# Kernel optimization log

Measured on AMD Instinct MI355X. Metric: run time of the kernel, lower is better.

The kernel has to match this reference:

```python
import jax, jax.numpy as jnp
import numpy as np

B, L, D, H = 4, 2048, 1024, 16
HD = D // H
SCALE = 1.0 / (D / H) ** 0.5


def setup_inputs() -> dict:
    key = jax.random.key(0)
    ks = jax.random.split(key, 11)
    s = 1.0 / np.sqrt(D)
    return {
        "q": jax.random.normal(ks[0], (B, L, D), jnp.float32),
        "k": jax.random.normal(ks[1], (B, L, D), jnp.float32),
        "v": jax.random.normal(ks[2], (B, L, D), jnp.float32),
        "Wq": jax.random.normal(ks[3], (D, D), jnp.float32) * s,
        "bq": jnp.zeros((D,), jnp.float32),
        "Wk": jax.random.normal(ks[4], (D, D), jnp.float32) * s,
        "bk": jnp.zeros((D,), jnp.float32),
        "Wv": jax.random.normal(ks[5], (D, D), jnp.float32) * s,
        "bv": jnp.zeros((D,), jnp.float32),
        "Wo": jax.random.normal(ks[6], (D, D), jnp.float32) * s,
        "bo": jnp.zeros((D,), jnp.float32),
    }


def _split_heads(x):
    # [b, l, h*d] -> [b, h, l, d]
    b, l, _ = x.shape
    return x.reshape(b, l, H, HD).transpose(0, 2, 1, 3)


def reference(q, k, v, Wq, bq, Wk, bk, Wv, bv, Wo, bo):
    # Linear projections (torch Linear: x @ W.T + b)
    qh = _split_heads(q @ Wq.T + bq)            # [b, h, l, d]
    kh = _split_heads(k @ Wk.T + bk)            # [b, h, l, d]
    vh = _split_heads(v @ Wv.T + bv)            # [b, h, l, d]
    scores = jnp.einsum('bhqd,bhkd->bhqk', qh, kh) * SCALE
    attn = jax.nn.softmax(scores, axis=-1)       # dropout p=0 -> identity
    out = jnp.einsum('bhqk,bhkd->bhqd', attn, vh)
    out = out.transpose(0, 2, 1, 3).reshape(q.shape[0], q.shape[1], D)
    return out @ Wo.T + bo
```

## Files before the change

### kernel.cpp

```cpp
#include <hip/hip_runtime.h>


#define Bsz 4
#define Lq 2048
#define Dm 1024
#define NH 16
#define HD 64
#define QSCALE 0.18033688011112042f

typedef unsigned short u16;
typedef __attribute__((ext_vector_type(4))) short bf16x4;
typedef __attribute__((ext_vector_type(8))) short short8;
typedef __attribute__((ext_vector_type(4))) float f32x4;

#define MFMA32(a, b, c) __builtin_amdgcn_mfma_f32_16x16x32_bf16(a, b, c, 0, 0, 0)

typedef __attribute__((address_space(3))) unsigned su32;
typedef __attribute__((address_space(1))) unsigned gu32;
__device__ __forceinline__ void gl_lds16(const u16* g, u16* l) {
  __builtin_amdgcn_global_load_lds((gu32*)(g), (su32*)(l), 16, 0, 0);
}

__device__ __forceinline__ u16 f2b(float x) {
  unsigned u = __builtin_bit_cast(unsigned, x);
  return (u16)((u + 0x7fffu + ((u >> 16) & 1u)) >> 16);
}
__device__ __forceinline__ unsigned pk2(float a, float b) {
  return (unsigned)f2b(a) | ((unsigned)f2b(b) << 16);
}
__device__ __forceinline__ unsigned pk2p(float a, float b) {
  return __builtin_amdgcn_perm(__builtin_bit_cast(unsigned, b) + 0x8000u,
                               __builtin_bit_cast(unsigned, a) + 0x8000u, 0x07060302u);
}
__device__ __forceinline__ float fexp2(float x) {
#if __has_builtin(__builtin_amdgcn_exp2f)
  return __builtin_amdgcn_exp2f(x);
#else
  return exp2f(x);
#endif
}

__global__ void castk3(const float* __restrict__ q, const float* __restrict__ k,
                       const float* __restrict__ v, u16* __restrict__ dst) {
  const float* s = blockIdx.y == 0 ? q : (blockIdx.y == 1 ? k : v);
  u16* d = dst + (size_t)blockIdx.y * (Bsz * Lq * Dm);
  int i = (blockIdx.x * 256 + threadIdx.x) * 8;
  float4 a = *(const float4*)(s + i);
  float4 b = *(const float4*)(s + i + 4);
  short8 o;
  o[0] = (short)f2b(a.x); o[1] = (short)f2b(a.y);
  o[2] = (short)f2b(a.z); o[3] = (short)f2b(a.w);
  o[4] = (short)f2b(b.x); o[5] = (short)f2b(b.y);
  o[6] = (short)f2b(b.z); o[7] = (short)f2b(b.w);
  *(short8*)(d + i) = o;
}

__global__ void castw(const float* __restrict__ s0, const float* __restrict__ s1,
                      const float* __restrict__ s2, const float* __restrict__ s3,
                      u16* __restrict__ d0, u16* __restrict__ d1,
                      u16* __restrict__ d2, u16* __restrict__ d3) {
  const float* s; u16* d; float sc = 1.0f;
  switch (blockIdx.y) {
    case 0: s = s0; d = d0; sc = QSCALE; break;
    case 1: s = s1; d = d1; break;
    case 2: s = s2; d = d2; break;
    default: s = s3; d = d3; break;
  }
  int i = (blockIdx.x * 256 + threadIdx.x) * 8;
  float4 a = *(const float4*)(s + i);
  float4 b = *(const float4*)(s + i + 4);
  short8 o;
  o[0] = (short)f2b(a.x * sc); o[1] = (short)f2b(a.y * sc);
  o[2] = (short)f2b(a.z * sc); o[3] = (short)f2b(a.w * sc);
  o[4] = (short)f2b(b.x * sc); o[5] = (short)f2b(b.y * sc);
  o[6] = (short)f2b(b.z * sc); o[7] = (short)f2b(b.w * sc);
  *(short8*)(d + i) = o;
}

__global__ __launch_bounds__(256) void qkv_gemm(
    const u16* __restrict__ Ab,
    const u16* __restrict__ Wqb, const u16* __restrict__ Wkb, const u16* __restrict__ Wvb,
    const float* __restrict__ bq, const float* __restrict__ bk, const float* __restrict__ bv,
    u16* __restrict__ Qh, u16* __restrict__ Kh, u16* __restrict__ Vtg)
{
  __shared__ __align__(16) u16 As[128 * 32];
  __shared__ __align__(16) u16 Bs[128 * 32];
  const int z = blockIdx.z;
  const u16* A  = Ab + (size_t)z * (Bsz * Lq * Dm);
  const u16* Bt = z == 0 ? Wqb : (z == 1 ? Wkb : Wvb);
  const float* bias = z == 0 ? bq : (z == 1 ? bk : bv);
  const float bscale = z == 0 ? QSCALE : 1.0f;

  const int tid  = threadIdx.x;
  const int lane = tid & 63;
  const int wave = tid >> 6;
  const int quad = lane >> 4;
  const int r16  = lane & 15;
  const int wm   = (wave >> 1) * 64;
  const int wn   = (wave & 1) * 64;
  const int m0   = blockIdx.y * 128;
  const int n0   = blockIdx.x * 128;

  const u16* ga = A  + (size_t)(m0 + wave * 32 + (lane >> 2)) * Dm + (lane & 3) * 8;
  const u16* gb = Bt + (size_t)(n0 + wave * 32 + (lane >> 2)) * Dm + (lane & 3) * 8;
  u16* la = As + wave * 1024;
  u16* lb = Bs + wave * 1024;

  f32x4 acc[4][4] = {};

  for (int k0 = 0; k0 < Dm; k0 += 32) {
    gl_lds16(ga + k0, la);
    gl_lds16(ga + k0 + 16 * Dm, la + 512);
    gl_lds16(gb + k0, lb);
    gl_lds16(gb + k0 + 16 * Dm, lb + 512);
    __syncthreads();

    short8 af[4], bfr[4];
#pragma unroll
    for (int mt = 0; mt < 4; ++mt) af[mt]  = *(const short8*)&As[(wm + mt * 16 + r16) * 32 + quad * 8];
#pragma unroll
    for (int nt = 0; nt < 4; ++nt) bfr[nt] = *(const short8*)&Bs[(wn + nt * 16 + r16) * 32 + quad * 8];
#pragma unroll
    for (int mt = 0; mt < 4; ++mt)
#pragma unroll
      for (int nt = 0; nt < 4; ++nt)
        acc[mt][nt] = MFMA32(af[mt], bfr[nt], acc[mt][nt]);
    __syncthreads();
  }

#pragma unroll
  for (int mt = 0; mt < 4; ++mt) {
#pragma unroll
    for (int nt = 0; nt < 4; ++nt) {
      int n = n0 + wn + nt * 16 + r16;
      float bv_ = bias[n] * bscale;
      if (z == 2) {
        int m_base = m0 + wm + mt * 16 + quad * 4;
        int b = m_base >> 11, l0 = m_base & 2047;
        int lp = (l0 & ~31) | (((l0 >> 2) & 3) << 3) | (((l0 >> 4) & 1) << 2);
        int h = n >> 6, d = n & 63;
        u16* dst = Vtg + (((size_t)(b * NH + h)) * HD + d) * Lq + lp;
        uint2 pkd;
        pkd.x = pk2(acc[mt][nt][0] + bv_, acc[mt][nt][1] + bv_);
        pkd.y = pk2(acc[mt][nt][2] + bv_, acc[mt][nt][3] + bv_);
        *(uint2*)dst = pkd;
      } else {
        u16* dst = z == 0 ? Qh : Kh;
#pragma unroll
        for (int j = 0; j < 4; ++j) {
          int m = m0 + wm + mt * 16 + quad * 4 + j;
          int b = m >> 11, l = m & 2047;
          int h = n >> 6,  d = n & 63;
          dst[(((size_t)(b * NH + h)) * Lq + l) * HD + d] = f2b(acc[mt][nt][j] + bv_);
        }
      }
    }
  }
}

__global__ __launch_bounds__(256) void gemm_wo(
    const u16* __restrict__ A, const u16* __restrict__ Bt,
    const float* __restrict__ bias, float* __restrict__ C)
{
  __shared__ __align__(16) u16 As[128 * 32];
  __shared__ __align__(16) u16 Bs[64 * 32];
  const int tid  = threadIdx.x;
  const int lane = tid & 63;
  const int wave = tid >> 6;
  const int quad = lane >> 4;
  const int r16  = lane & 15;
  const int wm   = wave * 32;
  const int m0   = blockIdx.y * 128;
  const int n0   = blockIdx.x * 64;

  const u16* ga = A  + (size_t)(m0 + wave * 32 + (lane >> 2)) * Dm + (lane & 3) * 8;
  const u16* gb = Bt + (size_t)(n0 + wave * 16 + (lane >> 2)) * Dm + (lane & 3) * 8;
  u16* la = As + wave * 1024;
  u16* lb = Bs + wave * 512;

  f32x4 acc[2][4] = {};

  for (int k0 = 0; k0 < Dm; k0 += 32) {
    gl_lds16(ga + k0, la);
    gl_lds16(ga + k0 + 16 * Dm, la + 512);
    gl_lds16(gb + k0, lb);
    __syncthreads();

    short8 af[2], bfr[4];
#pragma unroll
    for (int mt = 0; mt < 2; ++mt) af[mt]  = *(const short8*)&As[(wm + mt * 16 + r16) * 32 + quad * 8];
#pragma unroll
    for (int nt = 0; nt < 4; ++nt) bfr[nt] = *(const short8*)&Bs[(nt * 16 + r16) * 32 + quad * 8];
#pragma unroll
    for (int mt = 0; mt < 2; ++mt)
#pragma unroll
      for (int nt = 0; nt < 4; ++nt)
        acc[mt][nt] = MFMA32(af[mt], bfr[nt], acc[mt][nt]);
    __syncthreads();
  }

#pragma unroll
  for (int mt = 0; mt < 2; ++mt) {
#pragma unroll
    for (int nt = 0; nt < 4; ++nt) {
      int n = n0 + nt * 16 + r16;
      float bv = bias[n];
#pragma unroll
      for (int j = 0; j < 4; ++j) {
        int m = m0 + wm + mt * 16 + quad * 4 + j;
        C[(size_t)m * Dm + n] = acc[mt][nt][j] + bv;
      }
    }
  }
}

__global__ __launch_bounds__(256) void attn4(
    const u16* __restrict__ Qh, const u16* __restrict__ Kh,
    const u16* __restrict__ Vtg, u16* __restrict__ Oa)
{
  const int bh = blockIdx.y;
  const int qt = blockIdx.x;
  const int tid = threadIdx.x, lane = tid & 63, wave = tid >> 6;
  const int quad = lane >> 4, r16 = lane & 15;

  __shared__ __align__(16) u16 Ks[64][72];
  __shared__ __align__(16) u16 Vt[64][72];

  const int qbase = qt * 128 + wave * 32;
  short8 aq[2][2];
#pragma unroll
  for (int qf = 0; qf < 2; ++qf) {
    const size_t qrow = ((size_t)bh * Lq + qbase + qf * 16 + r16) * HD;
    aq[qf][0] = *(const short8*)(Qh + qrow + quad * 8);
    aq[qf][1] = *(const short8*)(Qh + qrow + 32 + quad * 8);
  }

  f32x4 oacc[2][4] = {};
  float lsum[2] = {0.f, 0.f};

  const int srow = tid >> 2;
  const int scid = (tid & 3) * 16;
  const u16* kg = Kh  + ((size_t)bh * Lq + srow) * HD + scid;
  const u16* vg = Vtg + ((size_t)bh * HD + srow) * Lq + scid;

  short8 pk0 = *(const short8*)(kg);
  short8 pk1 = *(const short8*)(kg + 8);
  short8 pv0 = *(const short8*)(vg);
  short8 pv1 = *(const short8*)(vg + 8);

  for (int t = 0; t < 32; ++t) {
    __syncthreads();
    *(short8*)&Ks[srow][scid]     = pk0;
    *(short8*)&Ks[srow][scid + 8] = pk1;
    *(short8*)&Vt[srow][scid]     = pv0;
    *(short8*)&Vt[srow][scid + 8] = pv1;
    __syncthreads();
    if (t < 31) {
      const u16* kgn = kg + (size_t)(t + 1) * 64 * HD;
      const u16* vgn = vg + (t + 1) * 64;
      pk0 = *(const short8*)(kgn);
      pk1 = *(const short8*)(kgn + 8);
      pv0 = *(const short8*)(vgn);
      pv1 = *(const short8*)(vgn + 8);
    }

#pragma unroll
    for (int ks = 0; ks < 2; ++ks) {
      f32x4 stq[2][2];
#pragma unroll
      for (int mtl = 0; mtl < 2; ++mtl) {
        const int mt = 2 * ks + mtl;
        short8 kf0 = *(const short8*)&Ks[mt * 16 + r16][quad * 8];
        short8 kf1 = *(const short8*)&Ks[mt * 16 + r16][32 + quad * 8];
#pragma unroll
        for (int qf = 0; qf < 2; ++qf) {
          f32x4 zz = {};
          zz = MFMA32(kf0, aq[qf][0], zz);
          zz = MFMA32(kf1, aq[qf][1], zz);
          stq[qf][mtl] = zz;
        }
      }
      short8 vf[4];
#pragma unroll
      for (int nt = 0; nt < 4; ++nt)
        vf[nt] = *(const short8*)&Vt[nt * 16 + r16][ks * 32 + quad * 8];
#pragma unroll
      for (int qf = 0; qf < 2; ++qf) {
        f32x4 sa = stq[qf][0], sb = stq[qf][1];
        float p0 = fexp2(sa[0]), p1 = fexp2(sa[1]), p2 = fexp2(sa[2]), p3 = fexp2(sa[3]);
        float p4 = fexp2(sb[0]), p5 = fexp2(sb[1]), p6 = fexp2(sb[2]), p7 = fexp2(sb[3]);
        lsum[qf] += ((p0 + p1) + (p2 + p3)) + ((p4 + p5) + (p6 + p7));
        uint4 pu;
        pu.x = pk2p(p0, p1);
        pu.y = pk2p(p2, p3);
        pu.z = pk2p(p4, p5);
        pu.w = pk2p(p6, p7);
        short8 pb = __builtin_bit_cast(short8, pu);
#pragma unroll
        for (int nt = 0; nt < 4; ++nt)
          oacc[qf][nt] = MFMA32(vf[nt], pb, oacc[qf][nt]);
      }
    }
  }

  const int b = bh >> 4, h = bh & 15;
  float linv[2];
#pragma unroll
  for (int qf = 0; qf < 2; ++qf) {
    float r = lsum[qf];
    r += __shfl_xor(r, 16);
    r += __shfl_xor(r, 32);
    linv[qf] = 1.0f / r;
  }
#pragma unroll
  for (int qf = 0; qf < 2; ++qf) {
    int q = qbase + qf * 16 + r16;
    size_t rowb = ((size_t)(b * Lq + q)) * Dm + h * HD;
#pragma unroll
    for (int nt = 0; nt < 4; ++nt) {
      f32x4 o = oacc[qf][nt];
      uint2 pkd;
      pkd.x = pk2(o[0] * linv[qf], o[1] * linv[qf]);
      pkd.y = pk2(o[2] * linv[qf], o[3] * linv[qf]);
      *(uint2*)&Oa[rowb + nt * 16 + quad * 4] = pkd;
    }
  }
}

extern "C" void kernel_launch(void* const* d_in, const int* in_sizes, int n_in,
                              void* d_out, int out_size, void* d_ws, size_t ws_size,
                              hipStream_t stream) {
  const float* q  = (const float*)d_in[0];
  const float* k  = (const float*)d_in[1];
  const float* v  = (const float*)d_in[2];
  const float* Wq = (const float*)d_in[3];
  const float* bq = (const float*)d_in[4];
  const float* Wk = (const float*)d_in[5];
  const float* bk = (const float*)d_in[6];
  const float* Wv = (const float*)d_in[7];
  const float* bv = (const float*)d_in[8];
  const float* Wo = (const float*)d_in[9];
  const float* bo = (const float*)d_in[10];

  const int NA = Bsz * Lq * Dm;
  u16* abuf = (u16*)d_ws;
  u16* Qh   = abuf + (size_t)3 * NA;
  u16* Kh   = Qh   + NA;
  u16* Vtg  = Kh   + NA;
  u16* wqb  = Vtg  + NA;
  u16* wkb  = wqb  + 1048576;
  u16* wvb  = wkb  + 1048576;
  u16* wob  = wvb  + 1048576;

  castw<<<dim3(512, 4), 256, 0, stream>>>(Wq, Wk, Wv, Wo, wqb, wkb, wvb, wob);
  castk3<<<dim3(NA / 2048, 3), 256, 0, stream>>>(q, k, v, abuf);

  qkv_gemm<<<dim3(8, 64, 3), 256, 0, stream>>>(abuf, wqb, wkb, wvb, bq, bk, bv, Qh, Kh, Vtg);

  attn4<<<dim3(Lq / 128, Bsz * NH), 256, 0, stream>>>(Qh, Kh, Vtg, abuf);

  gemm_wo<<<dim3(16, 64), 256, 0, stream>>>(abuf, wob, bo, (float*)d_out);
}
```

Measured before the change: 365.9 us.

## Swap MFMA operands for vectorized epilogues and compute row sums via MFMA

In the Q/K projection and the output GEMM, the MFMA operands are swapped so each lane holds four consecutive output columns. The epilogues can then issue vectorized stores (uint2 bf16 / float4) and vector bias loads in place of scalar strided writes. In attention, the softmax denominator is now accumulated with an extra MFMA against a ones vector instead of scalar adds and cross-lane shuffles. The extra MFMA per step adds matrix-core work, and the row sum now uses the bf16-rounded probabilities, which slightly changes numerics.

```diff
diff --git a/kernel.cpp b/kernel.cpp
--- a/kernel.cpp
+++ b/kernel.cpp
@@ -9,7 +9,6 @@
 #define QSCALE 0.18033688011112042f
 
 typedef unsigned short u16;
-typedef __attribute__((ext_vector_type(4))) short bf16x4;
 typedef __attribute__((ext_vector_type(8))) short short8;
 typedef __attribute__((ext_vector_type(4))) float f32x4;
 
@@ -108,51 +107,75 @@
 
   f32x4 acc[4][4] = {};
 
-  for (int k0 = 0; k0 < Dm; k0 += 32) {
-    gl_lds16(ga + k0, la);
-    gl_lds16(ga + k0 + 16 * Dm, la + 512);
-    gl_lds16(gb + k0, lb);
-    gl_lds16(gb + k0 + 16 * Dm, lb + 512);
-    __syncthreads();
-
-    short8 af[4], bfr[4];
-#pragma unroll
-    for (int mt = 0; mt < 4; ++mt) af[mt]  = *(const short8*)&As[(wm + mt * 16 + r16) * 32 + quad * 8];
-#pragma unroll
-    for (int nt = 0; nt < 4; ++nt) bfr[nt] = *(const short8*)&Bs[(wn + nt * 16 + r16) * 32 + quad * 8];
-#pragma unroll
-    for (int mt = 0; mt < 4; ++mt)
-#pragma unroll
-      for (int nt = 0; nt < 4; ++nt)
-        acc[mt][nt] = MFMA32(af[mt], bfr[nt], acc[mt][nt]);
-    __syncthreads();
-  }
-
-#pragma unroll
-  for (int mt = 0; mt < 4; ++mt) {
+  if (z < 2) {
+    for (int k0 = 0; k0 < Dm; k0 += 32) {
+      gl_lds16(ga + k0, la);
+      gl_lds16(ga + k0 + 16 * Dm, la + 512);
+      gl_lds16(gb + k0, lb);
+      gl_lds16(gb + k0 + 16 * Dm, lb + 512);
+      __syncthreads();
+      short8 af[4], bfr[4];
+#pragma unroll
+      for (int mt = 0; mt < 4; ++mt) af[mt]  = *(const short8*)&As[(wm + mt * 16 + r16) * 32 + quad * 8];
+#pragma unroll
+      for (int nt = 0; nt < 4; ++nt) bfr[nt] = *(const short8*)&Bs[(wn + nt * 16 + r16) * 32 + quad * 8];
+#pragma unroll
+      for (int mt = 0; mt < 4; ++mt)
+#pragma unroll
+        for (int nt = 0; nt < 4; ++nt)
+          acc[mt][nt] = MFMA32(bfr[nt], af[mt], acc[mt][nt]);
+      __syncthreads();
+    }
+    u16* dst = z == 0 ? Qh : Kh;
 #pragma unroll
     for (int nt = 0; nt < 4; ++nt) {
-      int n = n0 + wn + nt * 16 + r16;
-      float bv_ = bias[n] * bscale;
-      if (z == 2) {
+      const int nb = n0 + wn + nt * 16 + quad * 4;
+      float4 bv4 = *(const float4*)&bias[nb];
+      const int h = nb >> 6, d = nb & 63;
+#pragma unroll
+      for (int mt = 0; mt < 4; ++mt) {
+        const int l = m0 + wm + mt * 16 + r16;
+        const int b = l >> 11, lq = l & 2047;
+        uint2 pkd;
+        pkd.x = pk2(acc[mt][nt][0] + bv4.x * bscale, acc[mt][nt][1] + bv4.y * bscale);
+        pkd.y = pk2(acc[mt][nt][2] + bv4.z * bscale, acc[mt][nt][3] + bv4.w * bscale);
+        *(uint2*)&dst[(((size_t)(b * NH + h)) * Lq + lq) * HD + d] = pkd;
+      }
+    }
+  } else {
+    for (int k0 = 0; k0 < Dm; k0 += 32) {
+      gl_lds16(ga + k0, la);
+      gl_lds16(ga + k0 + 16 * Dm, la + 512);
+      gl_lds16(gb + k0, lb);
+      gl_lds16(gb + k0 + 16 * Dm, lb + 512);
+      __syncthreads();
+      short8 af[4], bfr[4];
+#pragma unroll
+      for (int mt = 0; mt < 4; ++mt) af[mt]  = *(const short8*)&As[(wm + mt * 16 + r16) * 32 + quad * 8];
+#pragma unroll
+      for (int nt = 0; nt < 4; ++nt) bfr[nt] = *(const short8*)&Bs[(wn + nt * 16 + r16) * 32 + quad * 8];
+#pragma unroll
+      for (int mt = 0; mt < 4; ++mt)
+#pragma unroll
+        for (int nt = 0; nt < 4; ++nt)
+          acc[mt][nt] = MFMA32(af[mt], bfr[nt], acc[mt][nt]);
+      __syncthreads();
+    }
+#pragma unroll
+    for (int mt = 0; mt < 4; ++mt) {
+#pragma unroll
+      for (int nt = 0; nt < 4; ++nt) {
+        int n = n0 + wn + nt * 16 + r16;
+        float bv_ = bias[n];
         int m_base = m0 + wm + mt * 16 + quad * 4;
         int b = m_base >> 11, l0 = m_base & 2047;
         int lp = (l0 & ~31) | (((l0 >> 2) & 3) << 3) | (((l0 >> 4) & 1) << 2);
         int h = n >> 6, d = n & 63;
-        u16* dst = Vtg + (((size_t)(b * NH + h)) * HD + d) * Lq + lp;
+        u16* dstv = Vtg + (((size_t)(b * NH + h)) * HD + d) * Lq + lp;
         uint2 pkd;
         pkd.x = pk2(acc[mt][nt][0] + bv_, acc[mt][nt][1] + bv_);
         pkd.y = pk2(acc[mt][nt][2] + bv_, acc[mt][nt][3] + bv_);
-        *(uint2*)dst = pkd;
-      } else {
-        u16* dst = z == 0 ? Qh : Kh;
-#pragma unroll
-        for (int j = 0; j < 4; ++j) {
-          int m = m0 + wm + mt * 16 + quad * 4 + j;
-          int b = m >> 11, l = m & 2047;
-          int h = n >> 6,  d = n & 63;
-          dst[(((size_t)(b * NH + h)) * Lq + l) * HD + d] = f2b(acc[mt][nt][j] + bv_);
-        }
+        *(uint2*)dstv = pkd;
       }
     }
   }
@@ -195,26 +218,28 @@
     for (int mt = 0; mt < 2; ++mt)
 #pragma unroll
       for (int nt = 0; nt < 4; ++nt)
-        acc[mt][nt] = MFMA32(af[mt], bfr[nt], acc[mt][nt]);
+        acc[mt][nt] = MFMA32(bfr[nt], af[mt], acc[mt][nt]);
     __syncthreads();
   }
 
 #pragma unroll
-  for (int mt = 0; mt < 2; ++mt) {
-#pragma unroll
-    for (int nt = 0; nt < 4; ++nt) {
-      int n = n0 + nt * 16 + r16;
-      float bv = bias[n];
-#pragma unroll
-      for (int j = 0; j < 4; ++j) {
-        int m = m0 + wm + mt * 16 + quad * 4 + j;
-        C[(size_t)m * Dm + n] = acc[mt][nt][j] + bv;
-      }
-    }
-  }
-}
-
-__global__ __launch_bounds__(256) void attn4(
+  for (int nt = 0; nt < 4; ++nt) {
+    const int nb = n0 + nt * 16 + quad * 4;
+    float4 bv4 = *(const float4*)&bias[nb];
+#pragma unroll
+    for (int mt = 0; mt < 2; ++mt) {
+      const int m = m0 + wm + mt * 16 + r16;
+      float4 o;
+      o.x = acc[mt][nt][0] + bv4.x;
+      o.y = acc[mt][nt][1] + bv4.y;
+      o.z = acc[mt][nt][2] + bv4.z;
+      o.w = acc[mt][nt][3] + bv4.w;
+      *(float4*)&C[(size_t)m * Dm + nb] = o;
+    }
+  }
+}
+
+__global__ __launch_bounds__(256) void attn5(
     const u16* __restrict__ Qh, const u16* __restrict__ Kh,
     const u16* __restrict__ Vtg, u16* __restrict__ Oa)
 {
@@ -236,7 +261,10 @@
   }
 
   f32x4 oacc[2][4] = {};
-  float lsum[2] = {0.f, 0.f};
+  f32x4 lacc[2] = {};
+  short8 ones8;
+#pragma unroll
+  for (int i = 0; i < 8; ++i) ones8[i] = (short)0x3F80;
 
   const int srow = tid >> 2;
   const int scid = (tid & 3) * 16;
@@ -289,13 +317,13 @@
         f32x4 sa = stq[qf][0], sb = stq[qf][1];
         float p0 = fexp2(sa[0]), p1 = fexp2(sa[1]), p2 = fexp2(sa[2]), p3 = fexp2(sa[3]);
         float p4 = fexp2(sb[0]), p5 = fexp2(sb[1]), p6 = fexp2(sb[2]), p7 = fexp2(sb[3]);
-        lsum[qf] += ((p0 + p1) + (p2 + p3)) + ((p4 + p5) + (p6 + p7));
         uint4 pu;
         pu.x = pk2p(p0, p1);
         pu.y = pk2p(p2, p3);
         pu.z = pk2p(p4, p5);
         pu.w = pk2p(p6, p7);
         short8 pb = __builtin_bit_cast(short8, pu);
+        lacc[qf] = MFMA32(ones8, pb, lacc[qf]);
 #pragma unroll
         for (int nt = 0; nt < 4; ++nt)
           oacc[qf][nt] = MFMA32(vf[nt], pb, oacc[qf][nt]);
@@ -304,24 +332,17 @@
   }
 
   const int b = bh >> 4, h = bh & 15;
-  float linv[2];
 #pragma unroll
   for (int qf = 0; qf < 2; ++qf) {
-    float r = lsum[qf];
-    r += __shfl_xor(r, 16);
-    r += __shfl_xor(r, 32);
-    linv[qf] = 1.0f / r;
-  }
-#pragma unroll
-  for (int qf = 0; qf < 2; ++qf) {
+    float linv = 1.0f / lacc[qf][0];
     int q = qbase + qf * 16 + r16;
     size_t rowb = ((size_t)(b * Lq + q)) * Dm + h * HD;
 #pragma unroll
     for (int nt = 0; nt < 4; ++nt) {
       f32x4 o = oacc[qf][nt];
       uint2 pkd;
-      pkd.x = pk2(o[0] * linv[qf], o[1] * linv[qf]);
-      pkd.y = pk2(o[2] * linv[qf], o[3] * linv[qf]);
+      pkd.x = pk2(o[0] * linv, o[1] * linv);
+      pkd.y = pk2(o[2] * linv, o[3] * linv);
       *(uint2*)&Oa[rowb + nt * 16 + quad * 4] = pkd;
     }
   }
@@ -357,7 +378,7 @@
 
   qkv_gemm<<<dim3(8, 64, 3), 256, 0, stream>>>(abuf, wqb, wkb, wvb, bq, bk, bv, Qh, Kh, Vtg);
 
-  attn4<<<dim3(Lq / 128, Bsz * NH), 256, 0, stream>>>(Qh, Kh, Vtg, abuf);
+  attn5<<<dim3(Lq / 128, Bsz * NH), 256, 0, stream>>>(Qh, Kh, Vtg, abuf);
 
   gemm_wo<<<dim3(16, 64), 256, 0, stream>>>(abuf, wob, bo, (float*)d_out);
 }
```

Result: no change. 366.8 us (+0.2%).
